# Kernel optimization log

Hardware: AMD Instinct MI355X
Metric: run time of the kernel (lower is better)

The kernel has to match this reference:

```python
import jax, jax.numpy as jnp
import numpy as np

DIM = 768
N_HEADS = 12
HEAD_DIM = DIM // N_HEADS
MLP_MULT = 4
EPS = 1e-5


def setup_inputs() -> dict:
    key = jax.random.key(0)
    ks = jax.random.split(key, 8)
    B, T = 2, 4096
    s = lambda fan_in: 1.0 / np.sqrt(fan_in)
    return {
        "x": jax.random.normal(ks[0], (B, T, DIM), dtype=jnp.float32),
        "ln1_w": jnp.ones((DIM,), jnp.float32),
        "ln1_b": jnp.zeros((DIM,), jnp.float32),
        # weights stored as (in, out): y = x @ W + b (equivalent to torch Linear)
        "w_qkv": jax.random.normal(ks[1], (DIM, 3 * DIM), jnp.float32) * s(DIM),
        "w_proj": jax.random.normal(ks[2], (DIM, DIM), jnp.float32) * s(DIM),
        "b_proj": jnp.zeros((DIM,), jnp.float32),
        "ln2_w": jnp.ones((DIM,), jnp.float32),
        "ln2_b": jnp.zeros((DIM,), jnp.float32),
        "w1": jax.random.normal(ks[3], (DIM, MLP_MULT * DIM), jnp.float32) * s(DIM),
        "b1": jnp.zeros((MLP_MULT * DIM,), jnp.float32),
        "w2": jax.random.normal(ks[4], (MLP_MULT * DIM, DIM), jnp.float32) * s(MLP_MULT * DIM),
        "b2": jnp.zeros((DIM,), jnp.float32),
    }


def _layernorm(x, w, b):
    mean = jnp.mean(x, axis=-1, keepdims=True)
    var = jnp.var(x, axis=-1, keepdims=True)
    return w * (x - mean) * jax.lax.rsqrt(var + EPS) + b


def reference(x, ln1_w, ln1_b, w_qkv, w_proj, b_proj, ln2_w, ln2_b, w1, b1, w2, b2):
    B, T, C = x.shape
    scale = HEAD_DIM ** -0.5

    # --- attention sub-block (pre-LN) ---
    h = _layernorm(x, ln1_w, ln1_b)
    qkv = h @ w_qkv                               # [B, T, 3C]
    q, k, v = jnp.split(qkv, 3, axis=-1)
    to_heads = lambda t: t.reshape(B, T, N_HEADS, HEAD_DIM).transpose(0, 2, 1, 3)
    q, k, v = to_heads(q), to_heads(k), to_heads(v)  # [B, H, T, D]

    att = jnp.einsum("bhqd,bhkd->bhqk", q, k) * scale  # full T x T scores
    causal = jnp.tril(jnp.ones((T, T), dtype=bool))
    att = jnp.where(causal, att, -jnp.inf)
    att = jax.nn.softmax(att, axis=-1)
    y = jnp.einsum("bhqk,bhkd->bhqd", att, v)          # [B, H, T, D]
    y = y.transpose(0, 2, 1, 3).reshape(B, T, C)
    y = y @ w_proj + b_proj
    x = x + y

    # --- MLP sub-block (pre-LN) ---
    h = _layernorm(x, ln2_w, ln2_b)
    h = jax.nn.gelu(h @ w1 + b1, approximate=False)
    h = h @ w2 + b2
    return x + h
```

## Files before the change

### kernel.cpp

```cpp
#include <hip/hip_runtime.h>

typedef unsigned short u16;
typedef __attribute__((ext_vector_type(4))) unsigned short u16x4;
typedef __attribute__((ext_vector_type(8))) short short8;
typedef __attribute__((ext_vector_type(4))) float f32x4;
typedef __attribute__((ext_vector_type(16))) float f32x16;

#define MFMA32(a, b, c) __builtin_amdgcn_mfma_f32_32x32x16_bf16(a, b, c, 0, 0, 0)

__device__ __forceinline__ u16 f2bf(float f) {
  union { float f; unsigned u; } x; x.f = f;
  unsigned r = x.u + 0x7fffu + ((x.u >> 16) & 1u);
  return (u16)(r >> 16);
}

__device__ __forceinline__ unsigned cvt_pk_bf16(float lo, float hi) {
  unsigned r;
  asm("v_cvt_pk_bf16_f32 %0, %1, %2" : "=v"(r) : "v"(lo), "v"(hi));
  return r;
}

__device__ __forceinline__ float fexp2m8(float t) {
  union { int i; float f; } u;
  u.i = (int)__builtin_fmaf(t, 8388608.f, 997996889.f);
  return u.f;
}

__device__ __forceinline__ void load_lds16(const void* g, void* l) {
  __builtin_amdgcn_global_load_lds(
      (const __attribute__((address_space(1))) void*)g,
      (__attribute__((address_space(3))) void*)l,
      16, 0, 0);
}

__global__ __launch_bounds__(256) void transpose_k(const float* __restrict__ in,
                                                   u16* __restrict__ out,
                                                   int R, int C) {
  __shared__ float tile[32][33];
  const int tx = threadIdx.x & 31, ty = threadIdx.x >> 5;
  const int c0 = blockIdx.x * 32, r0 = blockIdx.y * 32;
#pragma unroll
  for (int i = 0; i < 4; ++i)
    tile[ty + i * 8][tx] = in[(size_t)(r0 + ty + i * 8) * C + c0 + tx];
  __syncthreads();
#pragma unroll
  for (int i = 0; i < 4; ++i)
    out[(size_t)(c0 + ty + i * 8) * R + r0 + tx] = f2bf(tile[tx][ty + i * 8]);
}

__global__ __launch_bounds__(256) void ln_k(const float* __restrict__ X,
                                            const float* __restrict__ w,
                                            const float* __restrict__ b,
                                            u16* __restrict__ O) {
  const int row = blockIdx.x;
  const float* xr = X + (size_t)row * 768;
  const int tid = threadIdx.x;
  float v0 = xr[tid], v1 = xr[tid + 256], v2 = xr[tid + 512];
  float s = v0 + v1 + v2;
  float s2 = v0 * v0 + v1 * v1 + v2 * v2;
#pragma unroll
  for (int m = 32; m; m >>= 1) { s += __shfl_xor(s, m); s2 += __shfl_xor(s2, m); }
  __shared__ float ps[4], ps2[4];
  if ((tid & 63) == 0) { ps[tid >> 6] = s; ps2[tid >> 6] = s2; }
  __syncthreads();
  s = ps[0] + ps[1] + ps[2] + ps[3];
  s2 = ps2[0] + ps2[1] + ps2[2] + ps2[3];
  const float mean = s * (1.f / 768.f);
  const float var = s2 * (1.f / 768.f) - mean * mean;
  const float rstd = rsqrtf(var + 1e-5f);
  u16* orow = O + (size_t)row * 768;
  orow[tid]       = f2bf((v0 - mean) * rstd * w[tid]       + b[tid]);
  orow[tid + 256] = f2bf((v1 - mean) * rstd * w[tid + 256] + b[tid + 256]);
  orow[tid + 512] = f2bf((v2 - mean) * rstd * w[tid + 512] + b[tid + 512]);
}

#define BM 128
#define BN 128
#define BKK 64

template <int EPI>
__global__ __launch_bounds__(256, 3) void gemm_k(
    const u16* __restrict__ A, const u16* __restrict__ Bt, int K, int N,
    const float* __restrict__ bias, const float* __restrict__ res,
    float* __restrict__ outF, u16* __restrict__ outB,
    u16* __restrict__ qout, u16* __restrict__ kout, u16* __restrict__ vout) {
  __shared__ __align__(16) u16 sA[BM * BKK];
  __shared__ __align__(16) u16 sB[BN * BKK];
  const int nTn = N / BN;
  const int nwg = gridDim.x;
  const int bid = ((int)blockIdx.x & 7) * (nwg >> 3) + ((int)blockIdx.x >> 3);
  const int tm = bid / nTn, tn = bid % nTn;
  const int m0 = tm * BM, n0 = tn * BN;
  const int tid = threadIdx.x, lane = tid & 63, wv = tid >> 6;
  const int wr = wv >> 1, wc = wv & 1;
  const int fr = lane & 15, fg = lane >> 4;

  const u16* aSrc[4];
  const u16* bSrc[4];
#pragma unroll
  for (int i = 0; i < 4; ++i) {
    int f = (i * 4 + wv) * 64 + lane;
    int r = f >> 3;
    int c = (f & 7) ^ (r & 7);
    aSrc[i] = A + (size_t)(m0 + r) * K + c * 8;
    bSrc[i] = Bt + (size_t)(n0 + r) * K + c * 8;
  }

  f32x4 acc[4][4];
#pragma unroll
  for (int m = 0; m < 4; ++m)
#pragma unroll
    for (int n = 0; n < 4; ++n) acc[m][n] = f32x4{0.f, 0.f, 0.f, 0.f};

  const int aswz = fr & 7;
  for (int kt = 0; kt < K; kt += BKK) {
#pragma unroll
    for (int i = 0; i < 4; ++i) {
      load_lds16(aSrc[i] + kt, (char*)sA + (i * 4 + wv) * 1024);
      load_lds16(bSrc[i] + kt, (char*)sB + (i * 4 + wv) * 1024);
    }
    __syncthreads();
#pragma unroll
    for (int ks = 0; ks < 2; ++ks) {
      const int c16 = (ks * 4 + fg) ^ aswz;
      short8 af[4], bf[4];
#pragma unroll
      for (int m = 0; m < 4; ++m)
        af[m] = *(const short8*)((const char*)sA +
                                 (((wr * 64 + m * 16 + fr) * 8 + c16) << 4));
#pragma unroll
      for (int n = 0; n < 4; ++n)
        bf[n] = *(const short8*)((const char*)sB +
                                 (((wc * 64 + n * 16 + fr) * 8 + c16) << 4));
#pragma unroll
      for (int m = 0; m < 4; ++m)
#pragma unroll
        for (int n = 0; n < 4; ++n)
          acc[m][n] =
              __builtin_amdgcn_mfma_f32_16x16x32_bf16(af[m], bf[n], acc[m][n], 0, 0, 0);
    }
    __syncthreads();
  }

#pragma unroll
  for (int m = 0; m < 4; ++m) {
    const int row = m0 + wr * 64 + m * 16 + fg * 4;
#pragma unroll
    for (int n = 0; n < 4; ++n) {
      const int col = n0 + wc * 64 + n * 16 + fr;
      f32x4 v = acc[m][n];
      if (EPI == 0) {
        const int part = (col >= 1536) ? 2 : (col >= 768 ? 1 : 0);
        const int cc = col - part * 768;
        const int hh = cc >> 6, dd = cc & 63;
        const int bb = row >> 12;
        const int t = row & 4095;
        const size_t bhh = (size_t)(bb * 12 + hh);
        if (part == 2) {
          const int ks_ = (t & 63) >> 4, h_ = (t >> 3) & 1, e0 = t & 7;
          u16x4 pk = {f2bf(v[0]), f2bf(v[1]), f2bf(v[2]), f2bf(v[3])};
          *(u16x4*)(vout + bhh * 262144 + (size_t)(t >> 6) * 4096 +
                    (size_t)(((ks_ << 2) + ((dd >> 5) << 1) + h_) * 256 +
                             (dd & 31) * 8 + e0)) = pk;
        } else if (part == 1) {
          const int ks_ = dd >> 4, h_ = (dd >> 3) & 1, e = dd & 7;
          u16* base = kout + bhh * 262144;
#pragma unroll
          for (int r = 0; r < 4; ++r) {
            const int t2 = t + r;
            base[(size_t)(t2 >> 6) * 4096 +
                 (size_t)((((ks_ << 2) + (((t2 & 63) >> 5) << 1) + h_) * 256) +
                          (t2 & 31) * 8 + e)] = f2bf(v[r]);
          }
        } else {
          const float qs = 0.18033688011112042f;
          u16* dst = qout + (bhh * 4096 + t) * 64 + dd;
#pragma unroll
          for (int r = 0; r < 4; ++r) dst[(size_t)r * 64] = f2bf(v[r] * qs);
        }
      } else if (EPI == 1) {
        const float bv = bias[col];
#pragma unroll
        for (int r = 0; r < 4; ++r)
          outF[(size_t)(row + r) * N + col] =
              v[r] + bv + res[(size_t)(row + r) * N + col];
      } else {
        const float bv = bias[col];
#pragma unroll
        for (int r = 0; r < 4; ++r) {
          float t = v[r] + bv;
          float g = 0.5f * t * (1.f + erff(t * 0.70710678118654752f));
          outB[(size_t)(row + r) * N + col] = f2bf(g);
        }
      }
    }
  }
}

__global__ __launch_bounds__(256, 4) void gemm64_k(
    const u16* __restrict__ A, const u16* __restrict__ Bt, int K, int N,
    const float* __restrict__ bias, const float* __restrict__ res,
    float* __restrict__ outF) {
  __shared__ __align__(16) u16 sA[128 * 64];
  __shared__ __align__(16) u16 sB[64 * 64];
  const int nTn = N / 64;
  const int nwg = gridDim.x;
  const int bid = ((int)blockIdx.x & 7) * (nwg >> 3) + ((int)blockIdx.x >> 3);
  const int tm = bid / nTn, tn = bid % nTn;
  const int m0 = tm * 128, n0 = tn * 64;
  const int tid = threadIdx.x, lane = tid & 63, wv = tid >> 6;
  const int fr = lane & 15, fg = lane >> 4;

  const u16* aSrc[4];
  const u16* bSrc[2];
#pragma unroll
  for (int i = 0; i < 4; ++i) {
    const int f = i * 256 + tid;
    const int r = f >> 3;
    const int c = (f & 7) ^ (r & 7);
    aSrc[i] = A + (size_t)(m0 + r) * K + c * 8;
  }
#pragma unroll
  for (int i = 0; i < 2; ++i) {
    const int f = i * 256 + tid;
    const int r = f >> 3;
    const int c = (f & 7) ^ (r & 7);
    bSrc[i] = Bt + (size_t)(n0 + r) * K + c * 8;
  }

  f32x4 acc[2][4];
#pragma unroll
  for (int m = 0; m < 2; ++m)
#pragma unroll
    for (int n = 0; n < 4; ++n) acc[m][n] = f32x4{0.f, 0.f, 0.f, 0.f};

  const int aswz = fr & 7;
  for (int kt = 0; kt < K; kt += 64) {
#pragma unroll
    for (int i = 0; i < 4; ++i)
      load_lds16(aSrc[i] + kt, (char*)sA + (i * 256 + tid) * 16);
#pragma unroll
    for (int i = 0; i < 2; ++i)
      load_lds16(bSrc[i] + kt, (char*)sB + (i * 256 + tid) * 16);
    __syncthreads();
#pragma unroll
    for (int ks = 0; ks < 2; ++ks) {
      const int c16 = (ks * 4 + fg) ^ aswz;
      short8 af[2], bf[4];
#pragma unroll
      for (int m = 0; m < 2; ++m)
        af[m] = *(const short8*)((const char*)sA +
                                 (((wv * 32 + m * 16 + fr) * 8 + c16) << 4));
#pragma unroll
      for (int n = 0; n < 4; ++n)
        bf[n] = *(const short8*)((const char*)sB +
                                 (((n * 16 + fr) * 8 + c16) << 4));
#pragma unroll
      for (int m = 0; m < 2; ++m)
#pragma unroll
        for (int n = 0; n < 4; ++n)
          acc[m][n] =
              __builtin_amdgcn_mfma_f32_16x16x32_bf16(af[m], bf[n], acc[m][n], 0, 0, 0);
    }
    __syncthreads();
  }

#pragma unroll
  for (int m = 0; m < 2; ++m) {
    const int row = m0 + wv * 32 + m * 16 + fg * 4;
#pragma unroll
    for (int n = 0; n < 4; ++n) {
      const int col = n0 + n * 16 + fr;
      const float bv = bias[col];
      f32x4 v = acc[m][n];
#pragma unroll
      for (int r = 0; r < 4; ++r)
        outF[(size_t)(row + r) * N + col] =
            v[r] + bv + res[(size_t)(row + r) * N + col];
    }
  }
}

__global__ __launch_bounds__(256) void attn_k(const u16* __restrict__ Q,
                                              const u16* __restrict__ Kb,
                                              const u16* __restrict__ Vt,
                                              u16* __restrict__ Y) {
  __shared__ __align__(16) u16 sK[2][8192];
  __shared__ __align__(16) u16 sV[2][8192];
  const int bid = blockIdx.x;
  const int qt = 31 - bid / 24;
  const int bh = bid % 24;
  const int bb = bh / 12, hh = bh - bb * 12;
  const int tid = threadIdx.x, lane = tid & 63, wv = tid >> 6;
  const int l31 = lane & 31, hi = lane >> 5;
  const int wq0 = qt * 128 + wv * 32;
  const int qG = wq0 + l31;
  const u16* Qh = Q + (size_t)bh * 4096 * 64;
  const u16* Kh = Kb + (size_t)bh * 262144;
  const u16* Vh = Vt + (size_t)bh * 262144;

  short8 qf[4];
#pragma unroll
  for (int ks = 0; ks < 4; ++ks)
    qf[ks] = *(const short8*)(Qh + (size_t)qG * 64 + ks * 16 + hi * 8);

  const short8 onesf = {(short)0x3F80, (short)0x3F80, (short)0x3F80,
                        (short)0x3F80, (short)0x3F80, (short)0x3F80,
                        (short)0x3F80, (short)0x3F80};

  f32x16 yacc[2];
  yacc[0] = (f32x16)0.f;
  yacc[1] = (f32x16)0.f;
  f32x16 lsum = (f32x16)0.f;

#define STAGE(buf, cc)                                                         \
  do {                                                                         \
    const u16* gk_ = Kh + (size_t)(cc)*8192;                                   \
    const u16* gv_ = Vh + (size_t)(cc)*8192;                                   \
    _Pragma("unroll") for (int i_ = 0; i_ < 4; ++i_) {                         \
      const int f_ = i_ * 256 + tid;                                           \
      load_lds16(gk_ + f_ * 8, (char*)sK[buf] + f_ * 16);                      \
      load_lds16(gv_ + f_ * 8, (char*)sV[buf] + f_ * 16);                      \
    }                                                                          \
  } while (0)

  const int nch = qt + 1;
  STAGE(0, 0);
  __syncthreads();

  const int rdBase = hi * 512 + l31 * 16;

  for (int c = 0; c < nch; ++c) {
    const int cur = c & 1;
    if (c + 1 < nch) STAGE(cur ^ 1, c + 1);

#pragma unroll
    for (int hf = 0; hf < 2; ++hf) {
      const int kb = c * 128 + hf * 64;
      if (kb <= wq0 + 31) {
        const char* sKb = (const char*)sK[cur] + hf * 8192;
        const char* sVb = (const char*)sV[cur] + hf * 8192;

        f32x16 s[2];
        s[0] = (f32x16)0.f;
        s[1] = (f32x16)0.f;
        __builtin_amdgcn_s_setprio(1);
#pragma unroll
        for (int ks = 0; ks < 4; ++ks) {
#pragma unroll
          for (int kc = 0; kc < 2; ++kc) {
            short8 kf = *(const short8*)(sKb + ks * 2048 + kc * 1024 + rdBase);
            s[kc] = MFMA32(kf, qf[ks], s[kc]);
          }
        }
        __builtin_amdgcn_s_setprio(0);

        if (kb + 63 > wq0) {
#pragma unroll
          for (int kc = 0; kc < 2; ++kc)
#pragma unroll
            for (int r = 0; r < 16; ++r) {
              const int key = kb + kc * 32 + (r & 3) + 8 * (r >> 2) + 4 * hi;
              if (key > qG) s[kc][r] = -110.f;
            }
        }

#pragma unroll
        for (int kc = 0; kc < 2; ++kc)
#pragma unroll
          for (int r = 0; r < 16; ++r)
            s[kc][r] = fexp2m8(s[kc][r]);

#pragma unroll
        for (int ks2 = 0; ks2 < 4; ++ks2) {
          const int kc = ks2 >> 1, rb = (ks2 & 1) * 8;
          unsigned W0 = cvt_pk_bf16(s[kc][rb + 0], s[kc][rb + 1]);
          unsigned W1 = cvt_pk_bf16(s[kc][rb + 2], s[kc][rb + 3]);
          unsigned W2 = cvt_pk_bf16(s[kc][rb + 4], s[kc][rb + 5]);
          unsigned W3 = cvt_pk_bf16(s[kc][rb + 6], s[kc][rb + 7]);
          asm("v_permlane32_swap_b32 %0, %1" : "+v"(W0), "+v"(W2));
          asm("v_permlane32_swap_b32 %0, %1" : "+v"(W1), "+v"(W3));
          union { unsigned w[4]; short8 v; } pb;
          pb.w[0] = W0; pb.w[1] = W1; pb.w[2] = W2; pb.w[3] = W3;
          __builtin_amdgcn_s_setprio(1);
#pragma unroll
          for (int dt = 0; dt < 2; ++dt) {
            short8 vf = *(const short8*)(sVb + ks2 * 2048 + dt * 1024 + rdBase);
            yacc[dt] = MFMA32(vf, pb.v, yacc[dt]);
          }
          lsum = MFMA32(onesf, pb.v, lsum);
          __builtin_amdgcn_s_setprio(0);
        }
      }
    }
    __syncthreads();
  }

  const float inv = 1.f / lsum[0];
  u16* Yr = Y + (size_t)(bb * 4096 + qt * 128 + wv * 32 + l31) * 768 + hh * 64;
#pragma unroll
  for (int dt = 0; dt < 2; ++dt)
#pragma unroll
    for (int g = 0; g < 4; ++g) {
      u16x4 pk = {f2bf(yacc[dt][g * 4 + 0] * inv), f2bf(yacc[dt][g * 4 + 1] * inv),
                  f2bf(yacc[dt][g * 4 + 2] * inv), f2bf(yacc[dt][g * 4 + 3] * inv)};
      *(u16x4*)(Yr + dt * 32 + g * 8 + hi * 4) = pk;
    }
#undef STAGE
}

extern "C" void kernel_launch(void* const* d_in, const int* in_sizes, int n_in,
                              void* d_out, int out_size, void* d_ws, size_t ws_size,
                              hipStream_t stream) {
  const float* x = (const float*)d_in[0];
  const float* ln1w = (const float*)d_in[1];
  const float* ln1b = (const float*)d_in[2];
  const float* wqkv = (const float*)d_in[3];
  const float* wproj = (const float*)d_in[4];
  const float* bproj = (const float*)d_in[5];
  const float* ln2w = (const float*)d_in[6];
  const float* ln2b = (const float*)d_in[7];
  const float* w1 = (const float*)d_in[8];
  const float* b1 = (const float*)d_in[9];
  const float* w2 = (const float*)d_in[10];
  const float* b2 = (const float*)d_in[11];
  float* out = (float*)d_out;
  char* ws = (char*)d_ws;

  const size_t SZ_ACT = (size_t)8192 * 768 * 2;
  u16* hbuf = (u16*)(ws);
  u16* qb = (u16*)(ws + SZ_ACT);
  u16* kb = (u16*)(ws + 2 * SZ_ACT);
  u16* vT = (u16*)(ws + 3 * SZ_ACT);
  u16* ybuf = (u16*)(ws + 4 * SZ_ACT);
  float* out1 = (float*)(ws + 5 * SZ_ACT);
  char* wsw = ws + 5 * SZ_ACT + (size_t)8192 * 768 * 4;
  u16* wqkvT = (u16*)(wsw);
  u16* wprojT = (u16*)(wsw + 3538944);
  u16* w1T = (u16*)(wsw + 3538944 + 1179648);
  u16* w2T = (u16*)(wsw + 3538944 + 1179648 + 4718592);
  u16* h3 = hbuf;
  u16* h2 = ybuf;

  transpose_k<<<dim3(2304 / 32, 768 / 32), 256, 0, stream>>>(wqkv, wqkvT, 768, 2304);
  transpose_k<<<dim3(768 / 32, 768 / 32), 256, 0, stream>>>(wproj, wprojT, 768, 768);
  transpose_k<<<dim3(3072 / 32, 768 / 32), 256, 0, stream>>>(w1, w1T, 768, 3072);
  transpose_k<<<dim3(768 / 32, 3072 / 32), 256, 0, stream>>>(w2, w2T, 3072, 768);

  ln_k<<<8192, 256, 0, stream>>>(x, ln1w, ln1b, hbuf);

  gemm_k<0><<<64 * (2304 / 128), 256, 0, stream>>>(hbuf, wqkvT, 768, 2304,
      nullptr, nullptr, nullptr, nullptr, qb, kb, vT);

  attn_k<<<768, 256, 0, stream>>>(qb, kb, vT, ybuf);

  gemm64_k<<<64 * (768 / 64), 256, 0, stream>>>(ybuf, wprojT, 768, 768,
      bproj, x, out1);

  ln_k<<<8192, 256, 0, stream>>>(out1, ln2w, ln2b, h2);

  gemm_k<2><<<64 * (3072 / 128), 256, 0, stream>>>(h2, w1T, 768, 3072,
      b1, nullptr, nullptr, h3, nullptr, nullptr, nullptr);

  gemm64_k<<<64 * (768 / 64), 256, 0, stream>>>(h3, w2T, 3072, 768,
      b2, out1, out);

  (void)in_sizes; (void)n_in; (void)out_size; (void)ws_size;
}
```

Measured before the change: 267.9 us.

## Fuse weight transposes with LN1, read V from global, reorder attention blocks

```diff
diff --git a/kernel.cpp b/kernel.cpp
--- a/kernel.cpp
+++ b/kernel.cpp
@@ -33,19 +33,56 @@
       16, 0, 0);
 }
 
-__global__ __launch_bounds__(256) void transpose_k(const float* __restrict__ in,
-                                                   u16* __restrict__ out,
-                                                   int R, int C) {
-  __shared__ float tile[32][33];
-  const int tx = threadIdx.x & 31, ty = threadIdx.x >> 5;
-  const int c0 = blockIdx.x * 32, r0 = blockIdx.y * 32;
-#pragma unroll
-  for (int i = 0; i < 4; ++i)
-    tile[ty + i * 8][tx] = in[(size_t)(r0 + ty + i * 8) * C + c0 + tx];
-  __syncthreads();
-#pragma unroll
-  for (int i = 0; i < 4; ++i)
-    out[(size_t)(c0 + ty + i * 8) * R + r0 + tx] = f2bf(tile[tx][ty + i * 8]);
+__global__ __launch_bounds__(256) void prep_k(
+    const float* __restrict__ wqkv, const float* __restrict__ wproj,
+    const float* __restrict__ w1, const float* __restrict__ w2,
+    u16* __restrict__ wqkvT, u16* __restrict__ wprojT,
+    u16* __restrict__ w1T, u16* __restrict__ w2T,
+    const float* __restrict__ x, const float* __restrict__ ln1w,
+    const float* __restrict__ ln1b, u16* __restrict__ hbuf) {
+  __shared__ float smem[32 * 33];
+  const int bid = blockIdx.x;
+  const int tid = threadIdx.x;
+  if (bid < 6912) {
+    const float* in; u16* out; int C, tb;
+    int R;
+    if (bid < 1728)      { in = wqkv;  out = wqkvT;  R = 768;  C = 2304; tb = bid; }
+    else if (bid < 2304) { in = wproj; out = wprojT; R = 768;  C = 768;  tb = bid - 1728; }
+    else if (bid < 4608) { in = w1;    out = w1T;    R = 768;  C = 3072; tb = bid - 2304; }
+    else                 { in = w2;    out = w2T;    R = 3072; C = 768;  tb = bid - 4608; }
+    const int nCt = C >> 5;
+    const int c0 = (tb % nCt) * 32, r0 = (tb / nCt) * 32;
+    const int tx = tid & 31, ty = tid >> 5;
+    float (*tile)[33] = (float(*)[33])smem;
+#pragma unroll
+    for (int i = 0; i < 4; ++i)
+      tile[ty + i * 8][tx] = in[(size_t)(r0 + ty + i * 8) * C + c0 + tx];
+    __syncthreads();
+#pragma unroll
+    for (int i = 0; i < 4; ++i)
+      out[(size_t)(c0 + ty + i * 8) * R + r0 + tx] = f2bf(tile[tx][ty + i * 8]);
+  } else {
+    const int row = bid - 6912;
+    const float* xr = x + (size_t)row * 768;
+    float v0 = xr[tid], v1 = xr[tid + 256], v2 = xr[tid + 512];
+    float s = v0 + v1 + v2;
+    float s2 = v0 * v0 + v1 * v1 + v2 * v2;
+#pragma unroll
+    for (int m = 32; m; m >>= 1) { s += __shfl_xor(s, m); s2 += __shfl_xor(s2, m); }
+    float* ps = smem;
+    float* ps2 = smem + 4;
+    if ((tid & 63) == 0) { ps[tid >> 6] = s; ps2[tid >> 6] = s2; }
+    __syncthreads();
+    s = ps[0] + ps[1] + ps[2] + ps[3];
+    s2 = ps2[0] + ps2[1] + ps2[2] + ps2[3];
+    const float mean = s * (1.f / 768.f);
+    const float var = s2 * (1.f / 768.f) - mean * mean;
+    const float rstd = rsqrtf(var + 1e-5f);
+    u16* orow = hbuf + (size_t)row * 768;
+    orow[tid]       = f2bf((v0 - mean) * rstd * ln1w[tid]       + ln1b[tid]);
+    orow[tid + 256] = f2bf((v1 - mean) * rstd * ln1w[tid + 256] + ln1b[tid + 256]);
+    orow[tid + 512] = f2bf((v2 - mean) * rstd * ln1w[tid + 512] + ln1b[tid + 512]);
+  }
 }
 
 __global__ __launch_bounds__(256) void ln_k(const float* __restrict__ X,
@@ -281,15 +318,16 @@
   }
 }
 
-__global__ __launch_bounds__(256) void attn_k(const u16* __restrict__ Q,
-                                              const u16* __restrict__ Kb,
-                                              const u16* __restrict__ Vt,
-                                              u16* __restrict__ Y) {
+__global__ __launch_bounds__(256, 5) void attn_k(const u16* __restrict__ Q,
+                                                 const u16* __restrict__ Kb,
+                                                 const u16* __restrict__ Vt,
+                                                 u16* __restrict__ Y) {
   __shared__ __align__(16) u16 sK[2][8192];
-  __shared__ __align__(16) u16 sV[2][8192];
-  const int bid = blockIdx.x;
-  const int qt = 31 - bid / 24;
-  const int bh = bid % 24;
+  const int b = blockIdx.x;
+  const int c255 = b & 255, slot = b >> 8;
+  const int rank = (slot == 0) ? c255 : (slot == 1 ? 767 - c255 : 256 + c255);
+  const int qt = 31 - rank / 24;
+  const int bh = rank % 24;
   const int bb = bh / 12, hh = bh - bb * 12;
   const int tid = threadIdx.x, lane = tid & 63, wv = tid >> 6;
   const int l31 = lane & 31, hi = lane >> 5;
@@ -316,11 +354,9 @@
 #define STAGE(buf, cc)                                                         \
   do {                                                                         \
     const u16* gk_ = Kh + (size_t)(cc)*8192;                                   \
-    const u16* gv_ = Vh + (size_t)(cc)*8192;                                   \
     _Pragma("unroll") for (int i_ = 0; i_ < 4; ++i_) {                         \
       const int f_ = i_ * 256 + tid;                                           \
       load_lds16(gk_ + f_ * 8, (char*)sK[buf] + f_ * 16);                      \
-      load_lds16(gv_ + f_ * 8, (char*)sV[buf] + f_ * 16);                      \
     }                                                                          \
   } while (0)
 
@@ -329,6 +365,7 @@
   __syncthreads();
 
   const int rdBase = hi * 512 + l31 * 16;
+  const int vBase = hi * 256 + l31 * 8;
 
   for (int c = 0; c < nch; ++c) {
     const int cur = c & 1;
@@ -339,7 +376,7 @@
       const int kb = c * 128 + hf * 64;
       if (kb <= wq0 + 31) {
         const char* sKb = (const char*)sK[cur] + hf * 8192;
-        const char* sVb = (const char*)sV[cur] + hf * 8192;
+        const u16* vg = Vh + (size_t)c * 8192 + hf * 4096 + vBase;
 
         f32x16 s[2];
         s[0] = (f32x16)0.f;
@@ -385,7 +422,7 @@
           __builtin_amdgcn_s_setprio(1);
 #pragma unroll
           for (int dt = 0; dt < 2; ++dt) {
-            short8 vf = *(const short8*)(sVb + ks2 * 2048 + dt * 1024 + rdBase);
+            short8 vf = *(const short8*)(vg + ks2 * 1024 + dt * 512);
             yacc[dt] = MFMA32(vf, pb.v, yacc[dt]);
           }
           lsum = MFMA32(onesf, pb.v, lsum);
@@ -442,12 +479,9 @@
   u16* h3 = hbuf;
   u16* h2 = ybuf;
 
-  transpose_k<<<dim3(2304 / 32, 768 / 32), 256, 0, stream>>>(wqkv, wqkvT, 768, 2304);
-  transpose_k<<<dim3(768 / 32, 768 / 32), 256, 0, stream>>>(wproj, wprojT, 768, 768);
-  transpose_k<<<dim3(3072 / 32, 768 / 32), 256, 0, stream>>>(w1, w1T, 768, 3072);
-  transpose_k<<<dim3(768 / 32, 3072 / 32), 256, 0, stream>>>(w2, w2T, 3072, 768);
-
-  ln_k<<<8192, 256, 0, stream>>>(x, ln1w, ln1b, hbuf);
+  prep_k<<<15104, 256, 0, stream>>>(wqkv, wproj, w1, w2,
+                                    wqkvT, wprojT, w1T, w2T,
+                                    x, ln1w, ln1b, hbuf);
 
   gemm_k<0><<<64 * (2304 / 128), 256, 0, stream>>>(hbuf, wqkvT, 768, 2304,
       nullptr, nullptr, nullptr, nullptr, qb, kb, vT);
```

Result: slower. 413.7 us (+54.4%).
